# Kernel optimization log

Hardware: AMD Instinct MI355X
Metric: run time of the kernel (lower is better)

The kernel has to match this reference:

```python
import jax, jax.numpy as jnp
import numpy as np

# Band partition of the 2049 frequency bins (BSRNN-style: narrow low bands, wide high bands)
_WIDTHS = [25] * 10 + [50] * 12 + [100] * 8 + [399]
_STARTS = np.concatenate([[0], np.cumsum(_WIDTHS)])
SUBBANDS = [(int(_STARTS[i]), int(_STARTS[i + 1])) for i in range(len(_WIDTHS))]
C_IN = 2          # stereo complex input channels
OUT_CH = 128      # band embedding dim
EPS = 1e-5        # GroupNorm eps
TOTAL_CH = sum(2 * C_IN * (e - s) for s, e in SUBBANDS)  # 8196


def setup_inputs() -> dict:
    key = jax.random.key(0)
    k1, k2, k3, k4 = jax.random.split(key, 4)
    B, F, T = 8, 2049, 512
    # x is view_as_real of a complex spectrogram: [B, C, F, T, 2]
    x = jax.random.normal(k1, (B, C_IN, F, T), dtype=jnp.float32)
    x = jnp.stack([x, jax.random.normal(k2, (B, C_IN, F, T), dtype=jnp.float32)], axis=-1)
    gamma = jax.random.uniform(k3, (TOTAL_CH,), dtype=jnp.float32)            # GroupNorm weight (concat over bands)
    beta = jax.random.normal(k4, (TOTAL_CH,), dtype=jnp.float32) * 0.1       # GroupNorm bias
    W = jax.random.normal(jax.random.fold_in(key, 5), (OUT_CH, TOTAL_CH), dtype=jnp.float32) * 0.02  # 1x1 conv weights, concat over bands
    b = jax.random.normal(jax.random.fold_in(key, 6), (len(SUBBANDS), OUT_CH), dtype=jnp.float32) * 0.02
    return {"x": x, "gamma": gamma, "beta": beta, "W": W, "b": b}


def reference(x, gamma, beta, W, b):
    # x: [B, C, F, T, 2] (real view of complex spectrogram)
    B, C, F, T, _ = x.shape
    outs = []
    off = 0
    for i, (s, e) in enumerate(SUBBANDS):
        ch = 2 * C * (e - s)
        # moveaxis(-1, 1): [B, 2, C, w, T] -> reshape [B, 2*C*w, T]
        h = jnp.moveaxis(x[:, :, s:e, :, :], -1, 1).reshape(B, ch, T)
        # GroupNorm(1, ch): normalize over (channel, time) per sample
        mu = jnp.mean(h, axis=(1, 2), keepdims=True)
        var = jnp.var(h, axis=(1, 2), keepdims=True)
        g = gamma[off:off + ch][None, :, None]
        bt = beta[off:off + ch][None, :, None]
        hn = (h - mu) * jax.lax.rsqrt(var + EPS) * g + bt
        # 1x1 Conv1d == per-timestep linear: [out, ch] x [B, ch, T] -> [B, out, T]
        y = jnp.einsum('oc,bct->bot', W[:, off:off + ch], hn) + b[i][None, :, None]
        outs.append(y)
        off += ch
    return jnp.stack(outs, axis=2)  # [B, OUT_CH, n_bands, T]
```

## Files before the change

kernel.cpp:

```cpp
#include <hip/hip_runtime.h>
#include <hip/hip_bf16.h>

typedef __attribute__((ext_vector_type(8))) short short8;
typedef __attribute__((ext_vector_type(4))) float f32x4;

#define NBANDS 31
#define BB 8
#define CCH 2
#define FF 2049
#define TTS 512
#define OUTC 128
#define TCH 8196
#define EPSV 1e-5f

__constant__ int c_wid[NBANDS] = {
    25,25,25,25,25,25,25,25,25,25,
    50,50,50,50,50,50,50,50,50,50,50,50,
    100,100,100,100,100,100,100,100,
    399};
__constant__ int c_start[NBANDS] = {
    0,25,50,75,100,125,150,175,200,225,
    250,300,350,400,450,500,550,600,650,700,750,800,
    850,950,1050,1150,1250,1350,1450,1550,
    1650};
__constant__ int c_cumf[NBANDS + 1] = {
    0,1,2,3,4,5,6,7,8,9,
    10,12,14,16,18,20,22,24,26,28,30,32,
    34,38,42,46,50,54,58,62,
    66,79};
__constant__ int c_kpad[NBANDS] = {
    128,128,128,128,128,128,128,128,128,128,
    256,256,256,256,256,256,256,256,256,256,256,256,
    448,448,448,448,448,448,448,448,
    1600};
__constant__ int c_kbase[NBANDS] = {
    0,16384,32768,49152,65536,81920,98304,114688,131072,147456,
    163840,196608,229376,262144,294912,327680,360448,393216,425984,458752,491520,524288,
    557056,614400,671744,729088,786432,843776,901120,958464,
    1015808};
__constant__ int c_order[NBANDS] = {
    30,22,23,24,25,26,27,28,29,
    10,11,12,13,14,15,16,17,18,19,20,21,
    0,1,2,3,4,5,6,7,8,9};

#define NSTATS 1264
#define NWPREP 248
#define NWP2   992

__device__ inline unsigned short f2bf(float f) {
    __hip_bfloat16 h = __float2bfloat16(f);
    unsigned short u;
    __builtin_memcpy(&u, &h, 2);
    return u;
}

__device__ inline void gload_lds16(const void* g, void* l) {
    __builtin_amdgcn_global_load_lds((const __attribute__((address_space(1))) void*)g,
                                     (__attribute__((address_space(3))) void*)l, 16, 0, 0);
}

__global__ __launch_bounds__(256) void prep(const float* __restrict__ x,
                                            const float* __restrict__ W,
                                            const float* __restrict__ gamma,
                                            const float* __restrict__ beta,
                                            const float* __restrict__ bias,
                                            float* __restrict__ st,
                                            float* __restrict__ wgam,
                                            float* __restrict__ wcb,
                                            unsigned short* __restrict__ wgP) {
    __shared__ float s1[256], s2[256];
    const int bid = blockIdx.x;
    const int tid = threadIdx.x;

    if (bid < NSTATS) {
        int bx  = bid >> 4;
        int ycc = bid & 15;
        int band = 0;
        while (band + 1 < NBANDS && bx >= c_cumf[band + 1]) band++;
        int fc = bx - c_cumf[band];
        int b  = ycc >> 1;
        int cc = ycc & 1;
        int w = c_wid[band], s = c_start[band];
        int f0 = fc * 32;
        int rows = min(32, w - f0);

        const float4* p = (const float4*)(x + ((size_t)(b * CCH + cc) * FF + (s + f0)) * (TTS * 2));
        int n4 = rows * 256;
        float sum = 0.f, sq = 0.f;
        for (int i = tid; i < n4; i += 256) {
            float4 v = p[i];
            sum += v.x + v.y + v.z + v.w;
            sq  += v.x * v.x + v.y * v.y + v.z * v.z + v.w * v.w;
        }
        s1[tid] = sum; s2[tid] = sq;
        __syncthreads();
        for (int st_ = 128; st_ > 0; st_ >>= 1) {
            if (tid < st_) { s1[tid] += s1[tid + st_]; s2[tid] += s2[tid + st_]; }
            __syncthreads();
        }
        if (tid == 0) {
            float* dst = st + (size_t)(bx * 16 + ycc) * 2;
            dst[0] = s1[0];
            dst[1] = s2[0];
        }
    } else if (bid < NSTATS + NWPREP) {
        int r = bid - NSTATS;
        int band = r >> 3;
        int off = 4 * c_start[band];
        int ch  = 4 * c_wid[band];
        int o = (r & 7) * 16 + (tid >> 4);
        int lane = tid & 15;
        const float* wrow = W + (size_t)o * TCH + off;
        float sg = 0.f, sb = 0.f;
        for (int c = lane; c < ch; c += 16) {
            float wv = wrow[c];
            sg += wv * gamma[off + c];
            sb += wv * beta[off + c];
        }
        for (int m = 8; m; m >>= 1) {
            sg += __shfl_down(sg, m, 16);
            sb += __shfl_down(sb, m, 16);
        }
        if (lane == 0) {
            wgam[band * OUTC + o] = sg;
            wcb[band * OUTC + o]  = sb + bias[band * OUTC + o];
        }
    } else {
        int r = bid - (NSTATS + NWPREP);
        int band = r % NBANDS;
        int gy   = r / NBANDS;
        int w = c_wid[band];
        int s4 = 4 * c_start[band];
        int Kpad = c_kpad[band];
        int base = c_kbase[band];
        int K4 = 4 * w;
        int N = OUTC * Kpad;
        for (int idx = gy * 256 + tid; idx < N; idx += 32 * 256) {
            int o = idx / Kpad;
            int k = idx - o * Kpad;
            float val = 0.f;
            if (k < K4) {
                int ri = k & 1, p = k >> 1;
                int cc = (p >= w) ? 1 : 0;
                int f = p - cc * w;
                int c = s4 + ri * 2 * w + cc * w + f;
                val = W[(size_t)o * TCH + c] * gamma[c];
            }
            int slot = (k >> 3) & 7;
            int pos = (k >> 6) * 8192 + o * 64 + ((slot ^ (o & 7)) * 8) + (k & 7);
            wgP[base + pos] = f2bf(val);
        }
    }
}

__global__ __launch_bounds__(256, 4) void gemm_mfma(const float* __restrict__ x,
                                                 const unsigned short* __restrict__ wgP,
                                                 const float* __restrict__ st,
                                                 const float* __restrict__ wgam,
                                                 const float* __restrict__ wcb,
                                                 float* __restrict__ out) {
    const int band = c_order[blockIdx.y];
    const int b    = blockIdx.x >> 2;
    const int tt0  = (blockIdx.x & 3) * 128;
    const int w    = c_wid[band];
    const int s    = c_start[band];
    const int w2   = 2 * w;
    const int Kpad = c_kpad[band];
    const int nch  = Kpad >> 6;
    const unsigned short* wgA = wgP + c_kbase[band];

    __shared__ unsigned short lA[2][8192];

    const int tid  = threadIdx.x;
    const int lane = tid & 63;
    const int wv   = tid >> 6;
    const int l15  = lane & 15;
    const int lg   = lane >> 4;

    const float* xb = x + (size_t)b * (CCH * FF * TTS * 2);
    const float* colbase = xb + (size_t)(tt0 + wv * 32 + l15) * 2;

    f32x4 acc[8][2] = {};
    float2 bA[16];

#define LOADB(c, dst) do {                                                     \
    _Pragma("unroll")                                                          \
    for (int kk = 0; kk < 2; ++kk)                                             \
        _Pragma("unroll")                                                      \
        for (int nf = 0; nf < 2; ++nf)                                         \
            _Pragma("unroll")                                                  \
            for (int j = 0; j < 4; ++j) {                                      \
                int p = 32 * (c) + 16 * kk + 4 * lg + j;                       \
                p = min(p, w2 - 1);                                            \
                int row = s + p + ((p >= w) ? (FF - w) : 0);                   \
                dst[kk * 8 + nf * 4 + j] =                                     \
                    *(const float2*)(colbase + (size_t)row * 1024 + nf * 32);  \
            }                                                                  \
} while (0)

#define STAGE(c, buf) do {                                                     \
    const unsigned short* srcc = wgA + (size_t)(c) * 8192;                     \
    _Pragma("unroll")                                                          \
    for (int q = 0; q < 4; ++q)                                                \
        gload_lds16(srcc + q * 2048 + tid * 8, &lA[buf][q * 2048 + tid * 8]);  \
} while (0)

#define COMPUTE(br, buf) do {                                                  \
    _Pragma("unroll")                                                          \
    for (int kk = 0; kk < 2; ++kk) {                                           \
        short8 bf0, bf1;                                                       \
        _Pragma("unroll")                                                      \
        for (int j = 0; j < 4; ++j) {                                          \
            float2 v0 = br[kk * 8 + j];                                        \
            float2 v1 = br[kk * 8 + 4 + j];                                    \
            bf0[2 * j]     = (short)f2bf(v0.x);                                \
            bf0[2 * j + 1] = (short)f2bf(v0.y);                                \
            bf1[2 * j]     = (short)f2bf(v1.x);                                \
            bf1[2 * j + 1] = (short)f2bf(v1.y);                                \
        }                                                                      \
        _Pragma("unroll")                                                      \
        for (int m = 0; m < 8; ++m) {                                          \
            int o = m * 16 + l15;                                              \
            int slot = (lg + 4 * kk) ^ (o & 7);                                \
            short8 af = *(const short8*)&lA[buf][o * 64 + slot * 8];           \
            acc[m][0] = __builtin_amdgcn_mfma_f32_16x16x32_bf16(               \
                af, bf0, acc[m][0], 0, 0, 0);                                  \
            acc[m][1] = __builtin_amdgcn_mfma_f32_16x16x32_bf16(               \
                af, bf1, acc[m][1], 0, 0, 0);                                  \
        }                                                                      \
    }                                                                          \
} while (0)

    LOADB(0, bA);
    STAGE(0, 0);
    __syncthreads();
    for (int c = 0; c < nch; ++c) {
        if (c + 1 < nch) STAGE(c + 1, (c + 1) & 1);
        COMPUTE(bA, c & 1);
        if (c + 1 < nch) {
            LOADB(c + 1, bA);
            __syncthreads();
        }
    }
#undef LOADB
#undef STAGE
#undef COMPUTE

    float sum = 0.f, sq = 0.f;
    {
        int c0 = c_cumf[band], c1 = c_cumf[band + 1];
        for (int c = c0; c < c1; ++c) {
            const float* p0 = st + (size_t)(c * 16 + b * 2) * 2;
            sum += p0[0] + p0[2];
            sq  += p0[1] + p0[3];
        }
    }
    const float Nf = (float)(w * 2048);
    const float mu = sum / Nf;
    const float rs = rsqrtf(sq / Nf - mu * mu + EPSV);

#pragma unroll
    for (int m = 0; m < 8; ++m) {
#pragma unroll
        for (int r = 0; r < 4; ++r) {
            int o = m * 16 + lg * 4 + r;
            float wg = wgam[band * OUTC + o];
            float cb = wcb[band * OUTC + o];
            size_t rowoff = (((size_t)b * OUTC + o) * NBANDS + band) * TTS;
#pragma unroll
            for (int nf = 0; nf < 2; ++nf) {
                int t = tt0 + wv * 32 + nf * 16 + l15;
                out[rowoff + t] = rs * (acc[m][nf][r] - mu * wg) + cb;
            }
        }
    }
}

extern "C" void kernel_launch(void* const* d_in, const int* in_sizes, int n_in,
                              void* d_out, int out_size, void* d_ws, size_t ws_size,
                              hipStream_t stream) {
    const float* x     = (const float*)d_in[0];
    const float* gamma = (const float*)d_in[1];
    const float* beta  = (const float*)d_in[2];
    const float* W     = (const float*)d_in[3];
    const float* bias  = (const float*)d_in[4];
    float* out = (float*)d_out;
    float* ws  = (float*)d_ws;

    float* st_part = ws;
    float* wgam    = ws + 3072;
    float* wcb     = ws + 7168;
    unsigned short* wgP = (unsigned short*)(ws + 11264);

    prep<<<NSTATS + NWPREP + NWP2, 256, 0, stream>>>(x, W, gamma, beta, bias,
                                                     st_part, wgam, wcb, wgP);
    gemm_mfma<<<dim3(32, NBANDS), 256, 0, stream>>>(x, wgP, st_part, wgam, wcb, out);
}
```

Before: 97.87 us.

## Load weight fragments directly from global in MFMA layout, drop LDS staging

The prep kernel now writes the bf16 weights already arranged in per-lane MFMA fragment order, so the GEMM kernel reads A fragments straight from global memory (through cache) instead of staging them through double-buffered LDS with barriers. The B-operand register prefetch is now double-buffered with two register sets and the loop is unrolled by two, and occupancy hint drops to 3 blocks. This removes LDS traffic and __syncthreads but makes every wave reload the same weight data from L1/L2, and uses more registers.

```diff
diff --git a/kernel.cpp b/kernel.cpp
--- a/kernel.cpp
+++ b/kernel.cpp
@@ -54,11 +54,6 @@
     return u;
 }
 
-__device__ inline void gload_lds16(const void* g, void* l) {
-    __builtin_amdgcn_global_load_lds((const __attribute__((address_space(1))) void*)g,
-                                     (__attribute__((address_space(3))) void*)l, 16, 0, 0);
-}
-
 __global__ __launch_bounds__(256) void prep(const float* __restrict__ x,
                                             const float* __restrict__ W,
                                             const float* __restrict__ gamma,
@@ -146,19 +141,22 @@
                 int c = s4 + ri * 2 * w + cc * w + f;
                 val = W[(size_t)o * TCH + c] * gamma[c];
             }
-            int slot = (k >> 3) & 7;
-            int pos = (k >> 6) * 8192 + o * 64 + ((slot ^ (o & 7)) * 8) + (k & 7);
+            int chunk = k >> 6, k6 = k & 63;
+            int kk = k6 >> 5, kloc = k6 & 31;
+            int lg = kloc >> 3, j = kloc & 7;
+            int m = o >> 4, l15o = o & 15;
+            int pos = chunk * 8192 + kk * 4096 + m * 512 + (l15o + 16 * lg) * 8 + j;
             wgP[base + pos] = f2bf(val);
         }
     }
 }
 
-__global__ __launch_bounds__(256, 4) void gemm_mfma(const float* __restrict__ x,
-                                                 const unsigned short* __restrict__ wgP,
-                                                 const float* __restrict__ st,
-                                                 const float* __restrict__ wgam,
-                                                 const float* __restrict__ wcb,
-                                                 float* __restrict__ out) {
+__global__ __launch_bounds__(256, 3) void gemm_mfma(const float* __restrict__ x,
+                                                    const unsigned short* __restrict__ wgP,
+                                                    const float* __restrict__ st,
+                                                    const float* __restrict__ wgam,
+                                                    const float* __restrict__ wcb,
+                                                    float* __restrict__ out) {
     const int band = c_order[blockIdx.y];
     const int b    = blockIdx.x >> 2;
     const int tt0  = (blockIdx.x & 3) * 128;
@@ -167,9 +165,6 @@
     const int w2   = 2 * w;
     const int Kpad = c_kpad[band];
     const int nch  = Kpad >> 6;
-    const unsigned short* wgA = wgP + c_kbase[band];
-
-    __shared__ unsigned short lA[2][8192];
 
     const int tid  = threadIdx.x;
     const int lane = tid & 63;
@@ -177,11 +172,13 @@
     const int l15  = lane & 15;
     const int lg   = lane >> 4;
 
+    const unsigned short* apl = wgP + c_kbase[band] + lane * 8;
+
     const float* xb = x + (size_t)b * (CCH * FF * TTS * 2);
     const float* colbase = xb + (size_t)(tt0 + wv * 32 + l15) * 2;
 
     f32x4 acc[8][2] = {};
-    float2 bA[16];
+    float2 bA[16], bB[16];
 
 #define LOADB(c, dst) do {                                                     \
     _Pragma("unroll")                                                          \
@@ -198,16 +195,14 @@
             }                                                                  \
 } while (0)
 
-#define STAGE(c, buf) do {                                                     \
-    const unsigned short* srcc = wgA + (size_t)(c) * 8192;                     \
-    _Pragma("unroll")                                                          \
-    for (int q = 0; q < 4; ++q)                                                \
-        gload_lds16(srcc + q * 2048 + tid * 8, &lA[buf][q * 2048 + tid * 8]);  \
-} while (0)
-
-#define COMPUTE(br, buf) do {                                                  \
+#define COMPUTE(c, br) do {                                                    \
     _Pragma("unroll")                                                          \
     for (int kk = 0; kk < 2; ++kk) {                                           \
+        const unsigned short* ap = apl + (size_t)(c) * 8192 + kk * 4096;       \
+        short8 af[8];                                                          \
+        _Pragma("unroll")                                                      \
+        for (int m = 0; m < 8; ++m)                                            \
+            af[m] = *(const short8*)(ap + m * 512);                            \
         short8 bf0, bf1;                                                       \
         _Pragma("unroll")                                                      \
         for (int j = 0; j < 4; ++j) {                                          \
@@ -220,30 +215,24 @@
         }                                                                      \
         _Pragma("unroll")                                                      \
         for (int m = 0; m < 8; ++m) {                                          \
-            int o = m * 16 + l15;                                              \
-            int slot = (lg + 4 * kk) ^ (o & 7);                                \
-            short8 af = *(const short8*)&lA[buf][o * 64 + slot * 8];           \
             acc[m][0] = __builtin_amdgcn_mfma_f32_16x16x32_bf16(               \
-                af, bf0, acc[m][0], 0, 0, 0);                                  \
+                af[m], bf0, acc[m][0], 0, 0, 0);                               \
             acc[m][1] = __builtin_amdgcn_mfma_f32_16x16x32_bf16(               \
-                af, bf1, acc[m][1], 0, 0, 0);                                  \
+                af[m], bf1, acc[m][1], 0, 0, 0);                               \
         }                                                                      \
     }                                                                          \
 } while (0)
 
     LOADB(0, bA);
-    STAGE(0, 0);
-    __syncthreads();
-    for (int c = 0; c < nch; ++c) {
-        if (c + 1 < nch) STAGE(c + 1, (c + 1) & 1);
-        COMPUTE(bA, c & 1);
+    for (int c = 0; c < nch; c += 2) {
+        if (c + 1 < nch) LOADB(c + 1, bB);
+        COMPUTE(c, bA);
         if (c + 1 < nch) {
-            LOADB(c + 1, bA);
-            __syncthreads();
+            if (c + 2 < nch) LOADB(c + 2, bA);
+            COMPUTE(c + 1, bB);
         }
     }
 #undef LOADB
-#undef STAGE
 #undef COMPUTE
 
     float sum = 0.f, sq = 0.f;
```

Result: slower. 165.7 us (+69.3%).
